# Kernel optimization log

Measured on AMD Instinct MI355X. Metric: run time of the kernel, lower is better.

The kernel has to match this reference:

```python
import jax, jax.numpy as jnp
import numpy as np

D_MODEL = 1024
NUM_HEADS = 16
D_K = D_MODEL // NUM_HEADS  # 64
THETA = 10000.0
BATCH = 2
SEQ = 2048


def _rope_tables(positions, d_k, theta):
    # freq_k = theta**(-2k/d_k), each repeated twice (interleaved layout)
    k = jnp.arange(d_k // 2, dtype=jnp.float32)
    freq = theta ** (-2.0 * k / d_k)            # [d_k/2]
    freq = jnp.repeat(freq, 2)                  # [d_k], pattern f0,f0,f1,f1,...
    ang = positions.astype(jnp.float32)[:, None] * freq[None, :]  # [s, d_k]
    return jnp.cos(ang), jnp.sin(ang)


def _apply_rope(x, cos, sin):
    # x: [b, h, s, d_k]; interleaved rotation: y[0::2]=-x[1::2], y[1::2]=x[0::2]
    x1 = x[..., 0::2]
    x2 = x[..., 1::2]
    y = jnp.stack([-x2, x1], axis=-1).reshape(x.shape)
    return x * cos + y * sin


def setup_inputs() -> dict:
    key = jax.random.key(0)
    kx, kq, kk, kv, ko = jax.random.split(key, 5)
    sw = (2.0 / (2 * D_MODEL)) ** 0.5
    return {
        "x": jax.random.normal(kx, (BATCH, SEQ, D_MODEL), dtype=jnp.float32),
        "WQ": jax.random.normal(kq, (D_MODEL, D_MODEL), dtype=jnp.float32) * sw,
        "WK": jax.random.normal(kk, (D_MODEL, D_MODEL), dtype=jnp.float32) * sw,
        "WV": jax.random.normal(kv, (D_MODEL, D_MODEL), dtype=jnp.float32) * sw,
        "WO": jax.random.normal(ko, (D_MODEL, D_MODEL), dtype=jnp.float32) * sw,
        "token_positions": jnp.arange(SEQ, dtype=jnp.int32),
    }


def reference(x, WQ, WK, WV, WO, token_positions):
    b, s, d_model = x.shape
    h, d_k = NUM_HEADS, D_K

    # fused QKV projection: W = cat([WQ,WK,WV], 0); QKV = x @ W.T
    W = jnp.concatenate([WQ, WK, WV], axis=0)          # [3*d_model, d_model]
    QKV = jnp.einsum('bsd,ed->bse', x, W)              # [b, s, 3*d_model]
    Q, K, V = jnp.split(QKV, 3, axis=-1)               # each [b, s, d_model]

    def to_heads(t):
        return t.reshape(b, s, h, d_k).transpose(0, 2, 1, 3)  # [b, h, s, d_k]

    Q, K, V = to_heads(Q), to_heads(K), to_heads(V)

    cos, sin = _rope_tables(token_positions, d_k, THETA)       # [s, d_k]
    Q = _apply_rope(Q, cos, sin)
    K = _apply_rope(K, cos, sin)

    scale = 1.0 / jnp.sqrt(jnp.float32(d_k))
    scores = jnp.einsum('bhqd,bhkd->bhqk', Q, K) * scale       # [b,h,s,s]
    causal = jnp.tril(jnp.ones((s, s), dtype=bool))
    scores = jnp.where(causal[None, None], scores, -jnp.inf)
    probs = jax.nn.softmax(scores, axis=-1)
    attn = jnp.einsum('bhqk,bhkd->bhqd', probs, V)             # [b,h,s,d_k]
    attn = attn.transpose(0, 2, 1, 3).reshape(b, s, h * d_k)   # [b,s,d_model]
    return jnp.einsum('bsd,ed->bse', attn, WO)                 # [b,s,d_model]
```

## Files before the change

### kernel.cpp

```cpp
#include <hip/hip_runtime.h>
#include <hip/hip_bf16.h>
#include <math.h>

#define BATCH 2
#define SEQ 2048
#define DMODEL 1024
#define NHEADS 16
#define DK 64
#define BH (BATCH*NHEADS)
#define GK 1024

#define SCALE2 0.18033688011112042f
#define SHIFT  16.0f

typedef __bf16 bf16_t;
typedef __bf16 bf16x8 __attribute__((ext_vector_type(8)));
typedef __bf16 bf16x2 __attribute__((ext_vector_type(2)));
typedef float  floatx4 __attribute__((ext_vector_type(4)));

__device__ __forceinline__ void load_lds16(const bf16_t* g, bf16_t* l) {
    __builtin_amdgcn_global_load_lds(
        (const __attribute__((address_space(1))) void*)g,
        (__attribute__((address_space(3))) void*)l,
        16, 0, 0);
}

__global__ __launch_bounds__(256) void convert_all_kernel(
    const float* __restrict__ x,
    const float* __restrict__ WQ, const float* __restrict__ WK,
    const float* __restrict__ WV, const float* __restrict__ WO,
    bf16_t* __restrict__ xb, bf16_t* __restrict__ Wb)
{
    const int blk = blockIdx.x;
    const float* src;
    bf16_t* dst;
    int base;
    if (blk < 2048) {
        src = x; dst = xb; base = blk * 2048;
    } else {
        int wi  = (blk - 2048) >> 9;
        base = ((blk - 2048) & 511) * 2048;
        src = (wi == 0) ? WQ : (wi == 1) ? WK : (wi == 2) ? WV : WO;
        dst = Wb + (size_t)wi * DMODEL * DMODEL;
    }
    int i = base + threadIdx.x * 8;
    float4 a = *(const float4*)(src + i);
    float4 b = *(const float4*)(src + i + 4);
    bf16x8 o;
    o[0] = (bf16_t)a.x; o[1] = (bf16_t)a.y; o[2] = (bf16_t)a.z; o[3] = (bf16_t)a.w;
    o[4] = (bf16_t)b.x; o[5] = (bf16_t)b.y; o[6] = (bf16_t)b.z; o[7] = (bf16_t)b.w;
    *(bf16x8*)(dst + i) = o;
}

__device__ __forceinline__ void gemm128_mainloop(
    const bf16_t* __restrict__ Arows, const bf16_t* __restrict__ Brows,
    bf16_t (*As)[32], bf16_t (*Bs)[32], int tid, floatx4 acc[4][4])
{
    const int lane = tid & 63;
    const int w = tid >> 6;
    const int wm = w >> 1, wn = w & 1;
    const int r = lane & 15, q = lane >> 4;

    const int row0 = tid >> 2,         kc0 = (tid & 3) << 3;
    const int row1 = (tid + 256) >> 2, kc1 = kc0;

    for (int kt = 0; kt < GK; kt += 32) {
        __syncthreads();
        load_lds16(Arows + (size_t)row0 * GK + kt + kc0, &As[row0][kc0]);
        load_lds16(Arows + (size_t)row1 * GK + kt + kc1, &As[row1][kc1]);
        load_lds16(Brows + (size_t)row0 * GK + kt + kc0, &Bs[row0][kc0]);
        load_lds16(Brows + (size_t)row1 * GK + kt + kc1, &Bs[row1][kc1]);
        __syncthreads();

        bf16x8 af[4], bfr[4];
        #pragma unroll
        for (int i = 0; i < 4; ++i)
            af[i] = *(const bf16x8*)&As[wm * 64 + i * 16 + r][q << 3];
        #pragma unroll
        for (int j = 0; j < 4; ++j)
            bfr[j] = *(const bf16x8*)&Bs[wn * 64 + j * 16 + r][q << 3];

        #pragma unroll
        for (int i = 0; i < 4; ++i)
            #pragma unroll
            for (int j = 0; j < 4; ++j)
                acc[i][j] = __builtin_amdgcn_mfma_f32_16x16x32_bf16(
                    af[i], bfr[j], acc[i][j], 0, 0, 0);
    }
}

__global__ __launch_bounds__(256) void qkv_gemm_kernel(
    const bf16_t* __restrict__ x, const bf16_t* __restrict__ Wb,
    bf16_t* __restrict__ Qh, bf16_t* __restrict__ Kh, bf16_t* __restrict__ Vt)
{
    __shared__ __align__(16) bf16_t As[128][32];
    __shared__ __align__(16) bf16_t Bs[128][32];

    const int tid = threadIdx.x;
    const int m0 = blockIdx.y * 128;
    const int n0g = blockIdx.x * 128;
    const int which = n0g >> 10;
    const int nl0 = n0g & 1023;
    const bf16_t* Wsel = Wb + (size_t)which * DMODEL * DMODEL;

    floatx4 acc[4][4];
    #pragma unroll
    for (int i = 0; i < 4; ++i)
        #pragma unroll
        for (int j = 0; j < 4; ++j)
            acc[i][j] = (floatx4){0.f, 0.f, 0.f, 0.f};

    gemm128_mainloop(x + (size_t)m0 * GK, Wsel + (size_t)nl0 * GK, As, Bs, tid, acc);

    const int w = tid >> 6, lane = tid & 63;
    const int wm = w >> 1, wn = w & 1;
    const int r = lane & 15, q = lane >> 4;

    #pragma unroll
    for (int i = 0; i < 4; ++i) {
        #pragma unroll
        for (int j = 0; j < 4; ++j) {
            #pragma unroll
            for (int reg = 0; reg < 4; ++reg) {
                int m = m0 + wm * 64 + i * 16 + q * 4 + reg;
                int n = nl0 + wn * 64 + j * 16 + r;
                int h = n >> 6, dk = n & 63;
                int b = m >> 11, s = m & 2047;
                bf16_t v = (bf16_t)acc[i][j][reg];
                if (which == 0)
                    Qh[(((size_t)(b << 4) + h) * SEQ + s) * DK + dk] = v;
                else if (which == 1)
                    Kh[(((size_t)(b << 4) + h) * SEQ + s) * DK + dk] = v;
                else
                    Vt[(((size_t)(b << 4) + h) * DK + dk) * SEQ + s] = v;
            }
        }
    }
}

__global__ __launch_bounds__(256) void rope_apply_kernel(
    const int* __restrict__ pos, bf16_t* __restrict__ Qh, bf16_t* __restrict__ Kh)
{
    int idx = blockIdx.x * 256 + threadIdx.x;
    int kk = idx & 31;
    int row = idx >> 5;
    int s = row & (SEQ - 1);

    float freq = exp2f((float)kk * (-13.287712379549449f / 32.0f));
    float ang = (float)pos[s] * freq;
    float sn, cs;
    sincosf(ang, &sn, &cs);

    size_t off = (size_t)row * DK + (kk << 1);

    bf16x2 qp = *(bf16x2*)(Qh + off);
    float q0 = (float)qp[0], q1 = (float)qp[1];
    bf16x2 qo;
    qo[0] = (bf16_t)(q0 * cs - q1 * sn);
    qo[1] = (bf16_t)(q1 * cs + q0 * sn);
    *(bf16x2*)(Qh + off) = qo;

    bf16x2 kp = *(bf16x2*)(Kh + off);
    float k0 = (float)kp[0], k1 = (float)kp[1];
    bf16x2 ko;
    ko[0] = (bf16_t)(k0 * cs - k1 * sn);
    ko[1] = (bf16_t)(k1 * cs + k0 * sn);
    *(bf16x2*)(Kh + off) = ko;
}

__global__ __launch_bounds__(256) void attn_mfma_kernel(
    const bf16_t* __restrict__ Qh, const bf16_t* __restrict__ Kh,
    const bf16_t* __restrict__ Vtg, bf16_t* __restrict__ attnO)
{
    __shared__ __align__(16) bf16_t Ks[64][72];
    __shared__ __align__(16) bf16_t Vs[64][72];
    __shared__ __align__(16) bf16_t ps[4][16][72];

    const int tid = threadIdx.x, w = tid >> 6, lane = tid & 63;
    const int r = lane & 15, qd = lane >> 4;
    const int bh = blockIdx.y;

    const int row0 = tid >> 3,          c80 = (tid & 7) * 8;
    const int row1 = (tid + 256) >> 3,  c81 = c80;

    const bf16_t* Kbh = Kh  + (size_t)bh * SEQ * DK;
    const bf16_t* Vbh = Vtg + (size_t)bh * DK * SEQ;
    const int b = bh >> 4, h = bh & 15;

    #pragma unroll
    for (int half = 0; half < 2; ++half) {
        const int qt = half ? blockIdx.x : (31 - blockIdx.x);
        const int q0 = qt * 64;

        const bf16_t* Qbase = Qh + (((size_t)bh * SEQ) + q0 + w * 16 + r) * DK;
        bf16x8 aq0 = *(const bf16x8*)(Qbase + qd * 8);
        bf16x8 aq1 = *(const bf16x8*)(Qbase + 32 + qd * 8);

        bf16x8 pk0 = *(const bf16x8*)(Kbh + (size_t)row0 * DK + c80);
        bf16x8 pk1 = *(const bf16x8*)(Kbh + (size_t)row1 * DK + c81);
        bf16x8 pv0 = *(const bf16x8*)(Vbh + (size_t)row0 * SEQ + c80);
        bf16x8 pv1 = *(const bf16x8*)(Vbh + (size_t)row1 * SEQ + c81);

        floatx4 Oa[4];
        #pragma unroll
        for (int nd = 0; nd < 4; ++nd) Oa[nd] = (floatx4){0.f, 0.f, 0.f, 0.f};
        float l_lane[4] = {0.f, 0.f, 0.f, 0.f};

        for (int kb = 0; kb <= qt; ++kb) {
            __syncthreads();
            *(bf16x8*)&Ks[row0][c80] = pk0;
            *(bf16x8*)&Ks[row1][c81] = pk1;
            *(bf16x8*)&Vs[row0][c80] = pv0;
            *(bf16x8*)&Vs[row1][c81] = pv1;
            if (kb < qt) {
                const int j0n = (kb + 1) * 64;
                pk0 = *(const bf16x8*)(Kbh + (size_t)(j0n + row0) * DK + c80);
                pk1 = *(const bf16x8*)(Kbh + (size_t)(j0n + row1) * DK + c81);
                pv0 = *(const bf16x8*)(Vbh + (size_t)row0 * SEQ + j0n + c80);
                pv1 = *(const bf16x8*)(Vbh + (size_t)row1 * SEQ + j0n + c81);
            }
            __syncthreads();

            floatx4 acc[4];
            #pragma unroll
            for (int nt = 0; nt < 4; ++nt) {
                bf16x8 bk0 = *(const bf16x8*)&Ks[nt * 16 + r][qd * 8];
                bf16x8 bk1 = *(const bf16x8*)&Ks[nt * 16 + r][32 + qd * 8];
                floatx4 a = (floatx4){0.f, 0.f, 0.f, 0.f};
                a = __builtin_amdgcn_mfma_f32_16x16x32_bf16(aq0, bk0, a, 0, 0, 0);
                a = __builtin_amdgcn_mfma_f32_16x16x32_bf16(aq1, bk1, a, 0, 0, 0);
                acc[nt] = a;
            }

            const bool lastb = (kb == qt);
            #pragma unroll
            for (int nt = 0; nt < 4; ++nt)
                #pragma unroll
                for (int rg = 0; rg < 4; ++rg) {
                    float s2 = fmaf(acc[nt][rg], SCALE2, -SHIFT);
                    if (lastb && (nt * 16 + r > w * 16 + qd * 4 + rg)) s2 = -200.0f;
                    float p = exp2f(s2);
                    acc[nt][rg] = p;
                    l_lane[rg] += p;
                }

            #pragma unroll
            for (int nt = 0; nt < 4; ++nt)
                #pragma unroll
                for (int rg = 0; rg < 4; ++rg)
                    ps[w][qd * 4 + rg][nt * 16 + r] = (bf16_t)acc[nt][rg];
            bf16x8 ap0 = *(const bf16x8*)&ps[w][r][qd * 8];
            bf16x8 ap1 = *(const bf16x8*)&ps[w][r][32 + qd * 8];

            #pragma unroll
            for (int nd = 0; nd < 4; ++nd) {
                bf16x8 bv0 = *(const bf16x8*)&Vs[nd * 16 + r][qd * 8];
                bf16x8 bv1 = *(const bf16x8*)&Vs[nd * 16 + r][32 + qd * 8];
                floatx4 c = Oa[nd];
                c = __builtin_amdgcn_mfma_f32_16x16x32_bf16(ap0, bv0, c, 0, 0, 0);
                c = __builtin_amdgcn_mfma_f32_16x16x32_bf16(ap1, bv1, c, 0, 0, 0);
                Oa[nd] = c;
            }
        }

        float linv[4];
        #pragma unroll
        for (int rg = 0; rg < 4; ++rg) {
            float l = l_lane[rg];
            #pragma unroll
            for (int off = 1; off < 16; off <<= 1) l += __shfl_xor(l, off);
            linv[rg] = 1.0f / l;
        }

        #pragma unroll
        for (int rg = 0; rg < 4; ++rg) {
            int s = q0 + w * 16 + qd * 4 + rg;
            #pragma unroll
            for (int nd = 0; nd < 4; ++nd) {
                int d = nd * 16 + r;
                attnO[((size_t)b * SEQ + s) * DMODEL + (h << 6) + d] =
                    (bf16_t)(Oa[nd][rg] * linv[rg]);
            }
        }
    }
}

__global__ __launch_bounds__(256) void out_gemm_kernel(
    const bf16_t* __restrict__ attnI, const bf16_t* __restrict__ WOb,
    float* __restrict__ out)
{
    __shared__ __align__(16) bf16_t As[128][32];
    __shared__ __align__(16) bf16_t Bs[128][32];

    const int tid = threadIdx.x;
    const int m0 = blockIdx.y * 128;
    const int n0 = blockIdx.x * 128;

    floatx4 acc[4][4];
    #pragma unroll
    for (int i = 0; i < 4; ++i)
        #pragma unroll
        for (int j = 0; j < 4; ++j)
            acc[i][j] = (floatx4){0.f, 0.f, 0.f, 0.f};

    gemm128_mainloop(attnI + (size_t)m0 * GK, WOb + (size_t)n0 * GK, As, Bs, tid, acc);

    const int w = tid >> 6, lane = tid & 63;
    const int wm = w >> 1, wn = w & 1;
    const int r = lane & 15, q = lane >> 4;

    #pragma unroll
    for (int i = 0; i < 4; ++i) {
        #pragma unroll
        for (int j = 0; j < 4; ++j) {
            #pragma unroll
            for (int reg = 0; reg < 4; ++reg) {
                int m = m0 + wm * 64 + i * 16 + q * 4 + reg;
                int n = n0 + wn * 64 + j * 16 + r;
                out[(size_t)m * DMODEL + n] = acc[i][j][reg];
            }
        }
    }
}

extern "C" void kernel_launch(void* const* d_in, const int* in_sizes, int n_in,
                              void* d_out, int out_size, void* d_ws, size_t ws_size,
                              hipStream_t stream)
{
    (void)in_sizes; (void)n_in; (void)out_size; (void)ws_size;

    const float* x  = (const float*)d_in[0];
    const float* WQ = (const float*)d_in[1];
    const float* WK = (const float*)d_in[2];
    const float* WV = (const float*)d_in[3];
    const float* WO = (const float*)d_in[4];
    const int* tpos = (const int*)d_in[5];
    float* out = (float*)d_out;

    bf16_t* xb   = (bf16_t*)d_ws;
    bf16_t* Wb   = xb + (size_t)BATCH * SEQ * DMODEL;
    bf16_t* Qh   = Wb + (size_t)4 * DMODEL * DMODEL;
    bf16_t* Kh   = Qh + (size_t)BH * SEQ * DK;
    bf16_t* Vt   = Kh + (size_t)BH * SEQ * DK;
    bf16_t* attn = Vt + (size_t)BH * SEQ * DK;

    convert_all_kernel<<<dim3(4096), dim3(256), 0, stream>>>(
        x, WQ, WK, WV, WO, xb, Wb);

    qkv_gemm_kernel<<<dim3(3 * DMODEL / 128, BATCH * SEQ / 128), dim3(256), 0, stream>>>(
        xb, Wb, Qh, Kh, Vt);

    rope_apply_kernel<<<dim3(BH * SEQ * 32 / 256), dim3(256), 0, stream>>>(tpos, Qh, Kh);

    attn_mfma_kernel<<<dim3(16, 32), dim3(256), 0, stream>>>(Qh, Kh, Vt, attn);

    out_gemm_kernel<<<dim3(DMODEL / 128, BATCH * SEQ / 128), dim3(256), 0, stream>>>(
        attn, Wb + (size_t)3 * DMODEL * DMODEL, out);
}
```

Before: 208.1 us.

## Fuse RoPE into QKV GEMM epilogue and stage V transpose through LDS

Removes the separate RoPE pass over Q and K by applying the rotation in the QKV GEMM epilogue. The epilogue uses a lane shuffle to fetch the pair partner and reads cos/sin from a small precomputed table built by a new kernel. The V output is transposed through a padded LDS tile so it can be written to Vt with 16-byte coalesced stores instead of scattered 2-byte stores. The cost is about 34KB of extra LDS in the GEMM kernel, which may reduce occupancy, plus a table read per output element.

```diff
diff --git a/kernel.cpp b/kernel.cpp
--- a/kernel.cpp
+++ b/kernel.cpp
@@ -15,6 +15,7 @@
 
 typedef __bf16 bf16_t;
 typedef __bf16 bf16x8 __attribute__((ext_vector_type(8)));
+typedef __bf16 bf16x4 __attribute__((ext_vector_type(4)));
 typedef __bf16 bf16x2 __attribute__((ext_vector_type(2)));
 typedef float  floatx4 __attribute__((ext_vector_type(4)));
 
@@ -23,6 +24,18 @@
         (const __attribute__((address_space(1))) void*)g,
         (__attribute__((address_space(3))) void*)l,
         16, 0, 0);
+}
+
+__global__ __launch_bounds__(256) void rope_tables_kernel(
+    const int* __restrict__ pos, float2* __restrict__ csT)
+{
+    int idx = blockIdx.x * 256 + threadIdx.x;
+    int kk = idx & 31, s = idx >> 5;
+    float freq = exp2f((float)kk * (-13.287712379549449f / 32.0f));
+    float ang = (float)pos[s] * freq;
+    float sn, cs;
+    sincosf(ang, &sn, &cs);
+    csT[idx] = make_float2(cs, sn);
 }
 
 __global__ __launch_bounds__(256) void convert_all_kernel(
@@ -91,10 +104,12 @@
 
 __global__ __launch_bounds__(256) void qkv_gemm_kernel(
     const bf16_t* __restrict__ x, const bf16_t* __restrict__ Wb,
+    const float2* __restrict__ csT,
     bf16_t* __restrict__ Qh, bf16_t* __restrict__ Kh, bf16_t* __restrict__ Vt)
 {
     __shared__ __align__(16) bf16_t As[128][32];
     __shared__ __align__(16) bf16_t Bs[128][32];
+    __shared__ __align__(16) bf16_t Tt[128][136];
 
     const int tid = threadIdx.x;
     const int m0 = blockIdx.y * 128;
@@ -114,58 +129,55 @@
 
     const int w = tid >> 6, lane = tid & 63;
     const int wm = w >> 1, wn = w & 1;
-    const int r = lane & 15, q = lane >> 4;
-
-    #pragma unroll
-    for (int i = 0; i < 4; ++i) {
-        #pragma unroll
-        for (int j = 0; j < 4; ++j) {
-            #pragma unroll
-            for (int reg = 0; reg < 4; ++reg) {
-                int m = m0 + wm * 64 + i * 16 + q * 4 + reg;
-                int n = nl0 + wn * 64 + j * 16 + r;
-                int h = n >> 6, dk = n & 63;
-                int b = m >> 11, s = m & 2047;
-                bf16_t v = (bf16_t)acc[i][j][reg];
-                if (which == 0)
-                    Qh[(((size_t)(b << 4) + h) * SEQ + s) * DK + dk] = v;
-                else if (which == 1)
-                    Kh[(((size_t)(b << 4) + h) * SEQ + s) * DK + dk] = v;
-                else
-                    Vt[(((size_t)(b << 4) + h) * DK + dk) * SEQ + s] = v;
-            }
-        }
-    }
-}
-
-__global__ __launch_bounds__(256) void rope_apply_kernel(
-    const int* __restrict__ pos, bf16_t* __restrict__ Qh, bf16_t* __restrict__ Kh)
-{
-    int idx = blockIdx.x * 256 + threadIdx.x;
-    int kk = idx & 31;
-    int row = idx >> 5;
-    int s = row & (SEQ - 1);
-
-    float freq = exp2f((float)kk * (-13.287712379549449f / 32.0f));
-    float ang = (float)pos[s] * freq;
-    float sn, cs;
-    sincosf(ang, &sn, &cs);
-
-    size_t off = (size_t)row * DK + (kk << 1);
-
-    bf16x2 qp = *(bf16x2*)(Qh + off);
-    float q0 = (float)qp[0], q1 = (float)qp[1];
-    bf16x2 qo;
-    qo[0] = (bf16_t)(q0 * cs - q1 * sn);
-    qo[1] = (bf16_t)(q1 * cs + q0 * sn);
-    *(bf16x2*)(Qh + off) = qo;
-
-    bf16x2 kp = *(bf16x2*)(Kh + off);
-    float k0 = (float)kp[0], k1 = (float)kp[1];
-    bf16x2 ko;
-    ko[0] = (bf16_t)(k0 * cs - k1 * sn);
-    ko[1] = (bf16_t)(k1 * cs + k0 * sn);
-    *(bf16x2*)(Kh + off) = ko;
+    const int r = lane & 15, qd = lane >> 4;
+
+    if (which < 2) {
+        bf16_t* dst = (which == 0) ? Qh : Kh;
+        #pragma unroll
+        for (int i = 0; i < 4; ++i) {
+            #pragma unroll
+            for (int j = 0; j < 4; ++j) {
+                #pragma unroll
+                for (int reg = 0; reg < 4; ++reg) {
+                    int m = m0 + wm * 64 + i * 16 + qd * 4 + reg;
+                    int n = nl0 + wn * 64 + j * 16 + r;
+                    int h = n >> 6, dk = n & 63;
+                    int b = m >> 11, s = m & 2047;
+                    float v = acc[i][j][reg];
+                    float partner = __shfl_xor(v, 1);
+                    float2 cs = csT[(s << 5) + (dk >> 1)];
+                    float vr = ((n & 1) == 0) ? (v * cs.x - partner * cs.y)
+                                              : (v * cs.x + partner * cs.y);
+                    dst[(((size_t)(b << 4) + h) * SEQ + s) * DK + dk] = (bf16_t)vr;
+                }
+            }
+        }
+    } else {
+        #pragma unroll
+        for (int i = 0; i < 4; ++i) {
+            #pragma unroll
+            for (int j = 0; j < 4; ++j) {
+                int n_local = wn * 64 + j * 16 + r;
+                int m_base  = wm * 64 + i * 16 + qd * 4;
+                bf16x4 t;
+                #pragma unroll
+                for (int reg = 0; reg < 4; ++reg) t[reg] = (bf16_t)acc[i][j][reg];
+                *(bf16x4*)&Tt[n_local][m_base] = t;
+            }
+        }
+        __syncthreads();
+        const int b = m0 >> 11, s0 = m0 & 2047;
+        #pragma unroll
+        for (int k = 0; k < 8; ++k) {
+            int id = tid + 256 * k;
+            int row = id >> 4;
+            int ch  = id & 15;
+            int n = nl0 + row;
+            int h = n >> 6, dk = n & 63;
+            bf16x8 val = *(const bf16x8*)&Tt[row][ch * 8];
+            *(bf16x8*)(Vt + (((size_t)(b << 4) + h) * DK + dk) * SEQ + s0 + ch * 8) = val;
+        }
+    }
 }
 
 __global__ __launch_bounds__(256) void attn_mfma_kernel(
@@ -343,14 +355,15 @@
     bf16_t* Kh   = Qh + (size_t)BH * SEQ * DK;
     bf16_t* Vt   = Kh + (size_t)BH * SEQ * DK;
     bf16_t* attn = Vt + (size_t)BH * SEQ * DK;
+    float2* csT  = (float2*)(attn + (size_t)BATCH * SEQ * DMODEL);
+
+    rope_tables_kernel<<<dim3(SEQ * 32 / 256), dim3(256), 0, stream>>>(tpos, csT);
 
     convert_all_kernel<<<dim3(4096), dim3(256), 0, stream>>>(
         x, WQ, WK, WV, WO, xb, Wb);
 
     qkv_gemm_kernel<<<dim3(3 * DMODEL / 128, BATCH * SEQ / 128), dim3(256), 0, stream>>>(
-        xb, Wb, Qh, Kh, Vt);
-
-    rope_apply_kernel<<<dim3(BH * SEQ * 32 / 256), dim3(256), 0, stream>>>(tpos, Qh, Kh);
+        xb, Wb, csT, Qh, Kh, Vt);
 
     attn_mfma_kernel<<<dim3(16, 32), dim3(256), 0, stream>>>(Qh, Kh, Vt, attn);
 
```

After: 215.0 us. 3.3% more time.
